# Kernel optimization log

Measured on AMD Instinct MI355X. Metric: run time of the kernel, lower is better.

The kernel has to match this reference:

```python
import jax, jax.numpy as jnp
import numpy as np

N_NODES = 100000
N_EDGES = 1600000
D_IN, D_HID, D_OUT = 256, 512, 48
K_STEPS = 10
ALPHA = 0.1


def setup_inputs() -> dict:
    key = jax.random.key(0)
    k_x, k_e, k_w1, k_w2 = jax.random.split(key, 4)
    x = jax.random.normal(k_x, (N_NODES, D_IN), dtype=jnp.float32)
    edge_index = jax.random.randint(k_e, (2, N_EDGES), 0, N_NODES, dtype=jnp.int64)
    # MLP params (Kaiming-ish scaling)
    W1 = jax.random.normal(k_w1, (D_IN, D_HID), dtype=jnp.float32) * (1.0 / np.sqrt(D_IN))
    b1 = jnp.zeros((D_HID,), dtype=jnp.float32)
    W2 = jax.random.normal(k_w2, (D_HID, D_OUT), dtype=jnp.float32) * (1.0 / np.sqrt(D_HID))
    b2 = jnp.zeros((D_OUT,), dtype=jnp.float32)
    return {"x": x, "edge_index": edge_index, "W1": W1, "b1": b1, "W2": W2, "b2": b2}


def reference(x, edge_index, W1, b1, W2, b2):
    N = x.shape[0]
    # --- MLP encoder ---
    h = jax.nn.relu(x @ W1 + b1) @ W2 + b2  # [N, D_OUT]

    # --- APPNP propagation (PyG defaults: add self-loops, symmetric gcn_norm) ---
    loop = jnp.arange(N, dtype=edge_index.dtype)
    src = jnp.concatenate([edge_index[0], loop])  # [E+N]
    dst = jnp.concatenate([edge_index[1], loop])
    ones = jnp.ones(src.shape[0], dtype=h.dtype)
    deg = jax.ops.segment_sum(ones, dst, num_segments=N)  # in-degree incl. self-loop
    dinv = jnp.where(deg > 0, jax.lax.rsqrt(deg), 0.0)
    norm = dinv[src] * dinv[dst]  # [E+N]

    out = h
    for _ in range(K_STEPS):
        msg = out[src] * norm[:, None]                      # gather + scale
        agg = jax.ops.segment_sum(msg, dst, num_segments=N)  # scatter-add
        out = (1.0 - ALPHA) * agg + ALPHA * h                # teleport mix
    return out
```

## Files before the change

### kernel.cpp

```cpp
#include <hip/hip_runtime.h>
#include <hip/hip_fp16.h>

constexpr int D_IN = 256, D_HID = 512, D_OUT = 48;
constexpr int HPAD = 64;
constexpr int K_STEPS = 10;

typedef __attribute__((ext_vector_type(8))) __bf16 bf16x8;
typedef __attribute__((ext_vector_type(4))) float f32x4;

__device__ __forceinline__ unsigned short f2bf(float f) {
  unsigned u = __builtin_bit_cast(unsigned, f);
  u += 0x7fffu + ((u >> 16) & 1u);
  return (unsigned short)(u >> 16);
}

__device__ __forceinline__ void gl2lds16(const unsigned short* g, unsigned short* l) {
  __builtin_amdgcn_global_load_lds(
      (const __attribute__((address_space(1))) unsigned int*)g,
      (__attribute__((address_space(3))) unsigned int*)l, 16, 0, 0);
}


__global__ void zero2_kernel(int* __restrict__ a, int* __restrict__ b, int N) {
  int i = blockIdx.x * 256 + threadIdx.x;
  if (i < N) { a[i] = 0; b[i] = 0; }
}

__global__ void count_kernel(const int* __restrict__ dst, int* __restrict__ cnt, int E) {
  int e = blockIdx.x * 256 + threadIdx.x;
  if (e < E) atomicAdd(&cnt[dst[e]], 1);
}

__global__ void dinv_kernel(const int* __restrict__ cnt, float* __restrict__ dinv, int N) {
  int n = blockIdx.x * 256 + threadIdx.x;
  if (n < N) dinv[n] = rsqrtf((float)(cnt[n] + 1));
}

__global__ void scan1_kernel(const int* __restrict__ cnt, int* __restrict__ row_ptr,
                             int* __restrict__ bsum, int N) {
  __shared__ int sd[256];
  int tid = threadIdx.x, b = blockIdx.x;
  int i0 = b * 1024 + tid * 4;
  int v[4];
#pragma unroll
  for (int m = 0; m < 4; ++m) v[m] = (i0 + m < N) ? ((cnt[i0 + m] + 3) & ~3) : 0;
  int s = v[0] + v[1] + v[2] + v[3];
  sd[tid] = s;
  __syncthreads();
  for (int off = 1; off < 256; off <<= 1) {
    int t = (tid >= off) ? sd[tid - off] : 0;
    __syncthreads();
    sd[tid] += t;
    __syncthreads();
  }
  int run = sd[tid] - s;
#pragma unroll
  for (int m = 0; m < 4; ++m) {
    if (i0 + m < N) row_ptr[i0 + m] = run;
    run += v[m];
  }
  if (tid == 255) bsum[b] = sd[255];
}

__global__ void scan2_kernel(const int* __restrict__ bsum, int* __restrict__ bofs,
                             int* __restrict__ row_ptr, int NB, int N) {
  __shared__ int sd[128];
  int tid = threadIdx.x;
  int v = (tid < NB) ? bsum[tid] : 0;
  sd[tid] = v;
  __syncthreads();
  for (int off = 1; off < 128; off <<= 1) {
    int t = (tid >= off) ? sd[tid - off] : 0;
    __syncthreads();
    sd[tid] += t;
    __syncthreads();
  }
  if (tid < NB) bofs[tid] = sd[tid] - v;
  if (tid == 127) row_ptr[N] = sd[127];
}

__global__ void scan3_kernel(int* __restrict__ row_ptr, const int* __restrict__ bofs, int N) {
  int b = blockIdx.x;
  if (b == 0) return;
  int add = bofs[b];
  int i0 = b * 1024 + threadIdx.x * 4;
#pragma unroll
  for (int m = 0; m < 4; ++m)
    if (i0 + m < N) row_ptr[i0 + m] += add;
}

__global__ void fill_kernel(const int* __restrict__ src, const int* __restrict__ dst,
                            const int* __restrict__ row_ptr, int* __restrict__ cnt2,
                            const float* __restrict__ dinv,
                            int2* __restrict__ edges, int E) {
  int e = blockIdx.x * 256 + threadIdx.x;
  if (e >= E) return;
  int s = src[e], d = dst[e];
  int p = row_ptr[d] + atomicAdd(&cnt2[d], 1);
  edges[p] = make_int2(s, __float_as_int(dinv[s]));
}

__global__ void pad_kernel(const int* __restrict__ cnt, const int* __restrict__ row_ptr,
                           int2* __restrict__ edges, int N) {
  int n = blockIdx.x * 256 + threadIdx.x;
  if (n >= N) return;
  int a = row_ptr[n] + cnt[n];
  int b = row_ptr[n + 1];
  for (int p = a; p < b; ++p) edges[p] = make_int2(n, 0);
}


__global__ void convert_w1(const float* __restrict__ W1, unsigned short* __restrict__ W1F) {
  int i = blockIdx.x * 256 + threadIdx.x;
  if (i >= D_HID * D_IN) return;
  int c = i >> 8, k = i & 255;
  int ct = c >> 6, tn = (c >> 4) & 3, l15 = c & 15;
  int kb = k >> 5, q = (k >> 3) & 3, j = k & 7;
  int lane = (q << 4) | l15;
  int dst = (((ct * 4 + tn) * 8 + kb) << 9) + lane * 8 + j;
  W1F[dst] = f2bf(W1[k * D_HID + c]);
}

__global__ void convert_w2(const float* __restrict__ W2, unsigned short* __restrict__ W2F) {
  int i = blockIdx.x * 256 + threadIdx.x;
  if (i >= D_OUT * D_HID) return;
  int n = i >> 9, k = i & 511;
  int ct = k >> 6, kk = (k >> 5) & 1, q = (k >> 3) & 3, j = k & 7;
  int tn = n >> 4, l15 = n & 15;
  int lane = (q << 4) | l15;
  int dst = (((ct * 2 + kk) * 3 + tn) << 9) + lane * 8 + j;
  W2F[dst] = f2bf(W2[k * D_OUT + n]);
}


__global__ __launch_bounds__(256, 3) void encoder_kernel(
    const float* __restrict__ x, const float* __restrict__ b1,
    const float* __restrict__ b2,
    const unsigned short* __restrict__ W1F,
    const unsigned short* __restrict__ W2F,
    __half* __restrict__ h2, int N) {
  __shared__ unsigned short sW1[16384];
  __shared__ unsigned short sHid[4][2][16][72];

  int tid = threadIdx.x;
  int w = tid >> 6, lane = tid & 63;
  int q = lane >> 4, l15 = lane & 15;
  int row0 = blockIdx.x * 128 + w * 32;

  uint4 axu[2][8];
#pragma unroll
  for (int mt = 0; mt < 2; ++mt) {
    int grow = row0 + mt * 16 + l15;
    bool rok = grow < N;
    const float* xr = x + (size_t)grow * D_IN;
#pragma unroll
    for (int jb = 0; jb < 8; ++jb) {
      float4 v0 = make_float4(0.f, 0.f, 0.f, 0.f), v1 = v0;
      if (rok) {
        v0 = *(const float4*)(xr + jb * 32 + q * 8);
        v1 = *(const float4*)(xr + jb * 32 + q * 8 + 4);
      }
      union { uint4 u; unsigned short s[8]; } uu;
      uu.s[0] = f2bf(v0.x); uu.s[1] = f2bf(v0.y); uu.s[2] = f2bf(v0.z); uu.s[3] = f2bf(v0.w);
      uu.s[4] = f2bf(v1.x); uu.s[5] = f2bf(v1.y); uu.s[6] = f2bf(v1.z); uu.s[7] = f2bf(v1.w);
      axu[mt][jb] = uu.u;
    }
  }

  f32x4 hacc[2][3];
#pragma unroll
  for (int mt = 0; mt < 2; ++mt)
#pragma unroll
    for (int t = 0; t < 3; ++t)
#pragma unroll
      for (int r = 0; r < 4; ++r) hacc[mt][t][r] = 0.f;

  for (int ct = 0; ct < 8; ++ct) {
    int c0 = ct * 64;
    __syncthreads();
    {
      const unsigned short* gsrc = W1F + ((size_t)ct << 14) + (w << 9) + lane * 8;
      unsigned short* ldst = &sW1[w << 9];
#pragma unroll
      for (int i = 0; i < 8; ++i)
        gl2lds16(gsrc + (i << 11), ldst + (i << 11));
    }
    __syncthreads();

    f32x4 acc[2][4];
#pragma unroll
    for (int mt = 0; mt < 2; ++mt)
#pragma unroll
      for (int t = 0; t < 4; ++t)
#pragma unroll
        for (int r = 0; r < 4; ++r) acc[mt][t][r] = 0.f;

    const unsigned short* sb = &sW1[lane * 8];
#pragma unroll
    for (int kb = 0; kb < 8; ++kb) {
      bf16x8 bq0 = *(const bf16x8*)(sb + (kb << 9));
      bf16x8 bq1 = *(const bf16x8*)(sb + (kb << 9) + 4096);
      bf16x8 bq2 = *(const bf16x8*)(sb + (kb << 9) + 8192);
      bf16x8 bq3 = *(const bf16x8*)(sb + (kb << 9) + 12288);
      bf16x8 a0 = __builtin_bit_cast(bf16x8, axu[0][kb]);
      bf16x8 a1 = __builtin_bit_cast(bf16x8, axu[1][kb]);
      acc[0][0] = __builtin_amdgcn_mfma_f32_16x16x32_bf16(a0, bq0, acc[0][0], 0, 0, 0);
      acc[1][0] = __builtin_amdgcn_mfma_f32_16x16x32_bf16(a1, bq0, acc[1][0], 0, 0, 0);
      acc[0][1] = __builtin_amdgcn_mfma_f32_16x16x32_bf16(a0, bq1, acc[0][1], 0, 0, 0);
      acc[1][1] = __builtin_amdgcn_mfma_f32_16x16x32_bf16(a1, bq1, acc[1][1], 0, 0, 0);
      acc[0][2] = __builtin_amdgcn_mfma_f32_16x16x32_bf16(a0, bq2, acc[0][2], 0, 0, 0);
      acc[1][2] = __builtin_amdgcn_mfma_f32_16x16x32_bf16(a1, bq2, acc[1][2], 0, 0, 0);
      acc[0][3] = __builtin_amdgcn_mfma_f32_16x16x32_bf16(a0, bq3, acc[0][3], 0, 0, 0);
      acc[1][3] = __builtin_amdgcn_mfma_f32_16x16x32_bf16(a1, bq3, acc[1][3], 0, 0, 0);
    }
#pragma unroll
    for (int mt = 0; mt < 2; ++mt)
#pragma unroll
      for (int tn = 0; tn < 4; ++tn) {
        int c = tn * 16 + l15;
        float bias = b1[c0 + c];
#pragma unroll
        for (int rg = 0; rg < 4; ++rg) {
          float v = acc[mt][tn][rg] + bias;
          v = v > 0.f ? v : 0.f;
          sHid[w][mt][q * 4 + rg][c] = f2bf(v);
        }
      }
#pragma unroll
    for (int kk = 0; kk < 2; ++kk) {
      bf16x8 a0 = *(const bf16x8*)&sHid[w][0][l15][kk * 32 + q * 8];
      bf16x8 a1 = *(const bf16x8*)&sHid[w][1][l15][kk * 32 + q * 8];
      const unsigned short* w2b = W2F + (((ct * 2 + kk) * 3) << 9) + lane * 8;
#pragma unroll
      for (int tn = 0; tn < 3; ++tn) {
        bf16x8 b = *(const bf16x8*)(w2b + (tn << 9));
        hacc[0][tn] = __builtin_amdgcn_mfma_f32_16x16x32_bf16(a0, b, hacc[0][tn], 0, 0, 0);
        hacc[1][tn] = __builtin_amdgcn_mfma_f32_16x16x32_bf16(a1, b, hacc[1][tn], 0, 0, 0);
      }
    }
  }
#pragma unroll
  for (int mt = 0; mt < 2; ++mt) {
#pragma unroll
    for (int tn = 0; tn < 3; ++tn) {
      int c = tn * 16 + l15;
      float bias = b2[c];
#pragma unroll
      for (int rg = 0; rg < 4; ++rg) {
        int gr = row0 + mt * 16 + q * 4 + rg;
        if (gr < N) h2[(size_t)gr * HPAD + c] = __float2half(hacc[mt][tn][rg] + bias);
      }
    }
#pragma unroll
    for (int rg = 0; rg < 4; ++rg) {
      int gr = row0 + mt * 16 + q * 4 + rg;
      if (gr < N) h2[(size_t)gr * HPAD + 48 + l15] = __float2half(0.f);
    }
  }
}


__global__ __launch_bounds__(256) void prop_kernel(
    const __half* __restrict__ cur, const __half* __restrict__ h2,
    const float* __restrict__ dinv, const int* __restrict__ row_ptr,
    const int2* __restrict__ edges, __half* __restrict__ nxt,
    float* __restrict__ outf, int N, int last) {
  int wid = (blockIdx.x * 256 + threadIdx.x) >> 6;
  int lane = threadIdx.x & 63;
  int half = lane >> 5;
  int slot = (lane >> 3) & 3;
  int s = lane & 7;
  int node = wid * 2 + half;
  bool nok = node < N;
  int p0 = 0, p1 = 0;
  if (nok) { int2 pp = *(const int2*)(row_ptr + node); p0 = pp.x; p1 = pp.y; }
  int d = p1 - p0;
  int dmax = max(d, __shfl_xor(d, 32));
  int nb = dmax >> 2;

  float acc[8];
#pragma unroll
  for (int i = 0; i < 8; ++i) acc[i] = 0.f;

  int p = p0 + slot;
  int2 e0 = make_int2(0, 0), e1 = make_int2(0, 0);
  if (nb > 0) e0 = edges[p];
  if (nb > 1) e1 = edges[p + 4];
  int b = 0;
  for (; b + 2 <= nb; b += 2) {
    int2 n0 = make_int2(0, 0), n1 = make_int2(0, 0);
    if (b + 2 < nb) n0 = edges[p + 8];
    if (b + 3 < nb) n1 = edges[p + 12];
    float w0 = (p < p1) ? __int_as_float(e0.y) : 0.f;
    float w1 = (p + 4 < p1) ? __int_as_float(e1.y) : 0.f;
    union { float4 f; __half2 h[4]; } u0, u1;
    u0.f = *(const float4*)(cur + ((size_t)e0.x << 6) + s * 8);
    u1.f = *(const float4*)(cur + ((size_t)e1.x << 6) + s * 8);
#pragma unroll
    for (int i = 0; i < 4; ++i) {
      float2 f0 = __half22float2(u0.h[i]);
      float2 f1 = __half22float2(u1.h[i]);
      acc[2 * i]     += w0 * f0.x + w1 * f1.x;
      acc[2 * i + 1] += w0 * f0.y + w1 * f1.y;
    }
    e0 = n0; e1 = n1; p += 8;
  }
  if (b < nb) {
    float w0 = (p < p1) ? __int_as_float(e0.y) : 0.f;
    union { float4 f; __half2 h[4]; } u0;
    u0.f = *(const float4*)(cur + ((size_t)e0.x << 6) + s * 8);
#pragma unroll
    for (int i = 0; i < 4; ++i) {
      float2 f0 = __half22float2(u0.h[i]);
      acc[2 * i]     += w0 * f0.x;
      acc[2 * i + 1] += w0 * f0.y;
    }
  }
#pragma unroll
  for (int i = 0; i < 8; ++i) {
    acc[i] += __int_as_float(__builtin_amdgcn_ds_swizzle(__float_as_int(acc[i]), 0x201F));
    acc[i] += __int_as_float(__builtin_amdgcn_ds_swizzle(__float_as_int(acc[i]), 0x401F));
  }
  if ((lane & 24) != 0 || !nok) return;
  float di = dinv[node];
  size_t base = ((size_t)node << 6) + s * 8;
  union { float4 f; __half2 h[4]; } us, uh;
  us.f = *(const float4*)(cur + base);
  uh.f = *(const float4*)(h2 + base);
  float dii = di * di;
  float outv[8];
#pragma unroll
  for (int i = 0; i < 4; ++i) {
    float2 sf = __half22float2(us.h[i]);
    float2 hf = __half22float2(uh.h[i]);
    outv[2 * i]     = 0.9f * (di * acc[2 * i]     + dii * sf.x) + 0.1f * hf.x;
    outv[2 * i + 1] = 0.9f * (di * acc[2 * i + 1] + dii * sf.y) + 0.1f * hf.y;
  }
  if (last) {
    if (s < 6) {
      float* op = outf + (size_t)node * D_OUT + s * 8;
      *(float4*)op       = make_float4(outv[0], outv[1], outv[2], outv[3]);
      *(float4*)(op + 4) = make_float4(outv[4], outv[5], outv[6], outv[7]);
    }
  } else {
    union { uint4 u4; __half2 h[4]; } o;
#pragma unroll
    for (int i = 0; i < 4; ++i) o.h[i] = __floats2half2_rn(outv[2 * i], outv[2 * i + 1]);
    *(uint4*)(nxt + base) = o.u4;
  }
}


extern "C" void kernel_launch(void* const* d_in, const int* in_sizes, int n_in,
                              void* d_out, int out_size, void* d_ws, size_t ws_size,
                              hipStream_t stream) {
  (void)n_in; (void)out_size; (void)ws_size;
  const float* x  = (const float*)d_in[0];
  const int*   ei = (const int*)d_in[1];
  const float* W1 = (const float*)d_in[2];
  const float* b1 = (const float*)d_in[3];
  const float* W2 = (const float*)d_in[4];
  const float* b2 = (const float*)d_in[5];
  const int N = in_sizes[0] / D_IN;
  const int E = in_sizes[1] / 2;
  const int* e_src = ei;
  const int* e_dst = ei + E;

  char* ws = (char*)d_ws;
  size_t off = 0;
  auto take = [&](size_t bytes) -> char* {
    char* p = ws + off;
    off += (bytes + 511) & ~(size_t)511;
    return p;
  };
  int* cnt      = (int*)take((size_t)N * 4);
  int* cnt2     = (int*)take((size_t)N * 4);
  float* dinv   = (float*)take((size_t)N * 4);
  int* row_ptr  = (int*)take((size_t)(N + 1) * 4);
  int* bsum     = (int*)take(1024);
  int* bofs     = (int*)take(1024);
  int2* edges   = (int2*)take(((size_t)E + 4 * (size_t)N) * 8);
  unsigned short* W1F = (unsigned short*)take((size_t)D_IN * D_HID * 2);
  unsigned short* W2F = (unsigned short*)take((size_t)D_HID * D_OUT * 2);
  __half* h2    = (__half*)take((size_t)N * HPAD * 2);
  __half* bufA  = (__half*)take((size_t)N * HPAD * 2);
  __half* bufB  = (__half*)d_out;
  float* outp   = (float*)d_out;

  int nb256 = (N + 255) / 256;
  int eb256 = (E + 255) / 256;
  int NB    = (N + 1023) / 1024;

  zero2_kernel<<<nb256, 256, 0, stream>>>(cnt, cnt2, N);
  count_kernel<<<eb256, 256, 0, stream>>>(e_dst, cnt, E);
  dinv_kernel<<<nb256, 256, 0, stream>>>(cnt, dinv, N);
  scan1_kernel<<<NB, 256, 0, stream>>>(cnt, row_ptr, bsum, N);
  scan2_kernel<<<1, 128, 0, stream>>>(bsum, bofs, row_ptr, NB, N);
  scan3_kernel<<<NB, 256, 0, stream>>>(row_ptr, bofs, N);
  fill_kernel<<<eb256, 256, 0, stream>>>(e_src, e_dst, row_ptr, cnt2, dinv, edges, E);
  pad_kernel<<<nb256, 256, 0, stream>>>(cnt, row_ptr, edges, N);

  convert_w1<<<(D_IN * D_HID + 255) / 256, 256, 0, stream>>>(W1, W1F);
  convert_w2<<<(D_HID * D_OUT + 255) / 256, 256, 0, stream>>>(W2, W2F);
  encoder_kernel<<<(N + 127) / 128, 256, 0, stream>>>(x, b1, b2, W1F, W2F, h2, N);

  int waves = (N + 1) / 2;
  int pblocks = (waves + 3) / 4;
  const __half* src = h2;
  __half* dst = bufA;
  for (int it = 1; it <= K_STEPS; ++it) {
    int last = (it == K_STEPS);
    prop_kernel<<<pblocks, 256, 0, stream>>>(src, h2, dinv, row_ptr, edges,
                                             dst, outp, N, last);
    src = dst;
    dst = (dst == bufA) ? bufB : bufA;
  }
}
```

Measured before the change: 713.4 us.

## Partition atomic CSR build by destination range and retile encoder to 512 threads

The count and fill kernels now use a fixed grid of 2048 blocks split into 8 teams. Each team scans every edge but only performs atomics for destinations in its own 4096-node band, to improve atomic locality in L2. The encoder switches to 512-thread blocks with one 16-row tile per wave, caches the biases in LDS, and preloads the first W1 chunk before the x loads. In exchange, every edge is read 8 times in count and fill, and the W1 reload now sits between barriers without a double buffer.

Measured after the change: 714.8 us. About the same (+0.2%).

```diff
diff --git a/kernel.cpp b/kernel.cpp
--- a/kernel.cpp
+++ b/kernel.cpp
@@ -26,9 +26,15 @@
   if (i < N) { a[i] = 0; b[i] = 0; }
 }
 
-__global__ void count_kernel(const int* __restrict__ dst, int* __restrict__ cnt, int E) {
-  int e = blockIdx.x * 256 + threadIdx.x;
-  if (e < E) atomicAdd(&cnt[dst[e]], 1);
+__global__ __launch_bounds__(256) void count_kernel(const int* __restrict__ dst,
+                                                    int* __restrict__ cnt, int E) {
+  int team = blockIdx.x & 7;
+  int bt = blockIdx.x >> 3;
+  int step = (gridDim.x >> 3) * 256;
+  for (int e = bt * 256 + threadIdx.x; e < E; e += step) {
+    int d = dst[e];
+    if (((d >> 12) & 7) == team) atomicAdd(&cnt[d], 1);
+  }
 }
 
 __global__ void dinv_kernel(const int* __restrict__ cnt, float* __restrict__ dinv, int N) {
@@ -89,15 +95,20 @@
     if (i0 + m < N) row_ptr[i0 + m] += add;
 }
 
-__global__ void fill_kernel(const int* __restrict__ src, const int* __restrict__ dst,
-                            const int* __restrict__ row_ptr, int* __restrict__ cnt2,
-                            const float* __restrict__ dinv,
-                            int2* __restrict__ edges, int E) {
-  int e = blockIdx.x * 256 + threadIdx.x;
-  if (e >= E) return;
-  int s = src[e], d = dst[e];
-  int p = row_ptr[d] + atomicAdd(&cnt2[d], 1);
-  edges[p] = make_int2(s, __float_as_int(dinv[s]));
+__global__ __launch_bounds__(256) void fill_kernel(
+    const int* __restrict__ src, const int* __restrict__ dst,
+    const int* __restrict__ row_ptr, int* __restrict__ cnt2,
+    const float* __restrict__ dinv, int2* __restrict__ edges, int E) {
+  int team = blockIdx.x & 7;
+  int bt = blockIdx.x >> 3;
+  int step = (gridDim.x >> 3) * 256;
+  for (int e = bt * 256 + threadIdx.x; e < E; e += step) {
+    int d = dst[e];
+    if (((d >> 12) & 7) != team) continue;
+    int s = src[e];
+    int p = row_ptr[d] + atomicAdd(&cnt2[d], 1);
+    edges[p] = make_int2(s, __float_as_int(dinv[s]));
+  }
 }
 
 __global__ void pad_kernel(const int* __restrict__ cnt, const int* __restrict__ row_ptr,
@@ -133,129 +144,127 @@
 }
 
 
-__global__ __launch_bounds__(256, 3) void encoder_kernel(
+__global__ __launch_bounds__(512, 4) void encoder_kernel(
     const float* __restrict__ x, const float* __restrict__ b1,
     const float* __restrict__ b2,
     const unsigned short* __restrict__ W1F,
     const unsigned short* __restrict__ W2F,
     __half* __restrict__ h2, int N) {
   __shared__ unsigned short sW1[16384];
-  __shared__ unsigned short sHid[4][2][16][72];
+  __shared__ unsigned short sHid[8][16][72];
+  __shared__ float sB1[512];
+  __shared__ float sB2[64];
 
   int tid = threadIdx.x;
   int w = tid >> 6, lane = tid & 63;
   int q = lane >> 4, l15 = lane & 15;
-  int row0 = blockIdx.x * 128 + w * 32;
-
-  uint4 axu[2][8];
-#pragma unroll
-  for (int mt = 0; mt < 2; ++mt) {
-    int grow = row0 + mt * 16 + l15;
-    bool rok = grow < N;
-    const float* xr = x + (size_t)grow * D_IN;
-#pragma unroll
-    for (int jb = 0; jb < 8; ++jb) {
-      float4 v0 = make_float4(0.f, 0.f, 0.f, 0.f), v1 = v0;
-      if (rok) {
-        v0 = *(const float4*)(xr + jb * 32 + q * 8);
-        v1 = *(const float4*)(xr + jb * 32 + q * 8 + 4);
-      }
-      union { uint4 u; unsigned short s[8]; } uu;
-      uu.s[0] = f2bf(v0.x); uu.s[1] = f2bf(v0.y); uu.s[2] = f2bf(v0.z); uu.s[3] = f2bf(v0.w);
-      uu.s[4] = f2bf(v1.x); uu.s[5] = f2bf(v1.y); uu.s[6] = f2bf(v1.z); uu.s[7] = f2bf(v1.w);
-      axu[mt][jb] = uu.u;
-    }
-  }
-
-  f32x4 hacc[2][3];
-#pragma unroll
-  for (int mt = 0; mt < 2; ++mt)
-#pragma unroll
-    for (int t = 0; t < 3; ++t)
-#pragma unroll
-      for (int r = 0; r < 4; ++r) hacc[mt][t][r] = 0.f;
+  int row0 = blockIdx.x * 128 + w * 16;
+
+  {
+    const unsigned short* gsrc = W1F + (w << 9) + lane * 8;
+    unsigned short* ldst = &sW1[w << 9];
+#pragma unroll
+    for (int i = 0; i < 4; ++i)
+      gl2lds16(gsrc + (i << 12), ldst + (i << 12));
+  }
+  sB1[tid] = b1[tid];
+  if (tid < 48) sB2[tid] = b2[tid];
+
+  int grow = row0 + l15;
+  bool rok = grow < N;
+  const float* xr = x + (size_t)grow * D_IN;
+  float4 xv[16];
+#pragma unroll
+  for (int jb = 0; jb < 8; ++jb) {
+    xv[2 * jb]     = rok ? *(const float4*)(xr + jb * 32 + q * 8)
+                         : make_float4(0.f, 0.f, 0.f, 0.f);
+    xv[2 * jb + 1] = rok ? *(const float4*)(xr + jb * 32 + q * 8 + 4)
+                         : make_float4(0.f, 0.f, 0.f, 0.f);
+  }
+  uint4 axu[8];
+#pragma unroll
+  for (int jb = 0; jb < 8; ++jb) {
+    union { uint4 u; unsigned short s[8]; } uu;
+    float4 v0 = xv[2 * jb], v1 = xv[2 * jb + 1];
+    uu.s[0] = f2bf(v0.x); uu.s[1] = f2bf(v0.y); uu.s[2] = f2bf(v0.z); uu.s[3] = f2bf(v0.w);
+    uu.s[4] = f2bf(v1.x); uu.s[5] = f2bf(v1.y); uu.s[6] = f2bf(v1.z); uu.s[7] = f2bf(v1.w);
+    axu[jb] = uu.u;
+  }
+
+  f32x4 hacc[3];
+#pragma unroll
+  for (int t = 0; t < 3; ++t)
+#pragma unroll
+    for (int r = 0; r < 4; ++r) hacc[t][r] = 0.f;
+
+  __syncthreads();
 
   for (int ct = 0; ct < 8; ++ct) {
     int c0 = ct * 64;
-    __syncthreads();
-    {
-      const unsigned short* gsrc = W1F + ((size_t)ct << 14) + (w << 9) + lane * 8;
-      unsigned short* ldst = &sW1[w << 9];
-#pragma unroll
-      for (int i = 0; i < 8; ++i)
-        gl2lds16(gsrc + (i << 11), ldst + (i << 11));
-    }
-    __syncthreads();
-
-    f32x4 acc[2][4];
-#pragma unroll
-    for (int mt = 0; mt < 2; ++mt)
-#pragma unroll
-      for (int t = 0; t < 4; ++t)
-#pragma unroll
-        for (int r = 0; r < 4; ++r) acc[mt][t][r] = 0.f;
+    f32x4 acc[4];
+#pragma unroll
+    for (int t = 0; t < 4; ++t)
+#pragma unroll
+      for (int r = 0; r < 4; ++r) acc[t][r] = 0.f;
 
     const unsigned short* sb = &sW1[lane * 8];
 #pragma unroll
     for (int kb = 0; kb < 8; ++kb) {
+      bf16x8 a = __builtin_bit_cast(bf16x8, axu[kb]);
       bf16x8 bq0 = *(const bf16x8*)(sb + (kb << 9));
       bf16x8 bq1 = *(const bf16x8*)(sb + (kb << 9) + 4096);
       bf16x8 bq2 = *(const bf16x8*)(sb + (kb << 9) + 8192);
       bf16x8 bq3 = *(const bf16x8*)(sb + (kb << 9) + 12288);
-      bf16x8 a0 = __builtin_bit_cast(bf16x8, axu[0][kb]);
-      bf16x8 a1 = __builtin_bit_cast(bf16x8, axu[1][kb]);
-      acc[0][0] = __builtin_amdgcn_mfma_f32_16x16x32_bf16(a0, bq0, acc[0][0], 0, 0, 0);
-      acc[1][0] = __builtin_amdgcn_mfma_f32_16x16x32_bf16(a1, bq0, acc[1][0], 0, 0, 0);
-      acc[0][1] = __builtin_amdgcn_mfma_f32_16x16x32_bf16(a0, bq1, acc[0][1], 0, 0, 0);
-      acc[1][1] = __builtin_amdgcn_mfma_f32_16x16x32_bf16(a1, bq1, acc[1][1], 0, 0, 0);
-      acc[0][2] = __builtin_amdgcn_mfma_f32_16x16x32_bf16(a0, bq2, acc[0][2], 0, 0, 0);
-      acc[1][2] = __builtin_amdgcn_mfma_f32_16x16x32_bf16(a1, bq2, acc[1][2], 0, 0, 0);
-      acc[0][3] = __builtin_amdgcn_mfma_f32_16x16x32_bf16(a0, bq3, acc[0][3], 0, 0, 0);
-      acc[1][3] = __builtin_amdgcn_mfma_f32_16x16x32_bf16(a1, bq3, acc[1][3], 0, 0, 0);
-    }
-#pragma unroll
-    for (int mt = 0; mt < 2; ++mt)
-#pragma unroll
-      for (int tn = 0; tn < 4; ++tn) {
-        int c = tn * 16 + l15;
-        float bias = b1[c0 + c];
-#pragma unroll
-        for (int rg = 0; rg < 4; ++rg) {
-          float v = acc[mt][tn][rg] + bias;
-          v = v > 0.f ? v : 0.f;
-          sHid[w][mt][q * 4 + rg][c] = f2bf(v);
-        }
+      acc[0] = __builtin_amdgcn_mfma_f32_16x16x32_bf16(a, bq0, acc[0], 0, 0, 0);
+      acc[1] = __builtin_amdgcn_mfma_f32_16x16x32_bf16(a, bq1, acc[1], 0, 0, 0);
+      acc[2] = __builtin_amdgcn_mfma_f32_16x16x32_bf16(a, bq2, acc[2], 0, 0, 0);
+      acc[3] = __builtin_amdgcn_mfma_f32_16x16x32_bf16(a, bq3, acc[3], 0, 0, 0);
+    }
+#pragma unroll
+    for (int tn = 0; tn < 4; ++tn) {
+      int c = tn * 16 + l15;
+      float bias = sB1[c0 + c];
+#pragma unroll
+      for (int rg = 0; rg < 4; ++rg) {
+        float v = acc[tn][rg] + bias;
+        v = v > 0.f ? v : 0.f;
+        sHid[w][q * 4 + rg][c] = f2bf(v);
       }
+    }
 #pragma unroll
     for (int kk = 0; kk < 2; ++kk) {
-      bf16x8 a0 = *(const bf16x8*)&sHid[w][0][l15][kk * 32 + q * 8];
-      bf16x8 a1 = *(const bf16x8*)&sHid[w][1][l15][kk * 32 + q * 8];
+      bf16x8 a0 = *(const bf16x8*)&sHid[w][l15][kk * 32 + q * 8];
       const unsigned short* w2b = W2F + (((ct * 2 + kk) * 3) << 9) + lane * 8;
 #pragma unroll
       for (int tn = 0; tn < 3; ++tn) {
         bf16x8 b = *(const bf16x8*)(w2b + (tn << 9));
-        hacc[0][tn] = __builtin_amdgcn_mfma_f32_16x16x32_bf16(a0, b, hacc[0][tn], 0, 0, 0);
-        hacc[1][tn] = __builtin_amdgcn_mfma_f32_16x16x32_bf16(a1, b, hacc[1][tn], 0, 0, 0);
+        hacc[tn] = __builtin_amdgcn_mfma_f32_16x16x32_bf16(a0, b, hacc[tn], 0, 0, 0);
       }
     }
-  }
-#pragma unroll
-  for (int mt = 0; mt < 2; ++mt) {
-#pragma unroll
-    for (int tn = 0; tn < 3; ++tn) {
-      int c = tn * 16 + l15;
-      float bias = b2[c];
-#pragma unroll
-      for (int rg = 0; rg < 4; ++rg) {
-        int gr = row0 + mt * 16 + q * 4 + rg;
-        if (gr < N) h2[(size_t)gr * HPAD + c] = __float2half(hacc[mt][tn][rg] + bias);
-      }
-    }
+    __syncthreads();
+    if (ct < 7) {
+      const unsigned short* gsrc = W1F + ((size_t)(ct + 1) << 14) + (w << 9) + lane * 8;
+      unsigned short* ldst = &sW1[w << 9];
+#pragma unroll
+      for (int i = 0; i < 4; ++i)
+        gl2lds16(gsrc + (i << 12), ldst + (i << 12));
+      __syncthreads();
+    }
+  }
+#pragma unroll
+  for (int tn = 0; tn < 3; ++tn) {
+    int c = tn * 16 + l15;
+    float bias = sB2[c];
 #pragma unroll
     for (int rg = 0; rg < 4; ++rg) {
-      int gr = row0 + mt * 16 + q * 4 + rg;
-      if (gr < N) h2[(size_t)gr * HPAD + 48 + l15] = __float2half(0.f);
-    }
+      int gr = row0 + q * 4 + rg;
+      if (gr < N) h2[(size_t)gr * HPAD + c] = __float2half(hacc[tn][rg] + bias);
+    }
+  }
+#pragma unroll
+  for (int rg = 0; rg < 4; ++rg) {
+    int gr = row0 + q * 4 + rg;
+    if (gr < N) h2[(size_t)gr * HPAD + 48 + l15] = __float2half(0.f);
   }
 }
 
@@ -392,17 +401,17 @@
   int NB    = (N + 1023) / 1024;
 
   zero2_kernel<<<nb256, 256, 0, stream>>>(cnt, cnt2, N);
-  count_kernel<<<eb256, 256, 0, stream>>>(e_dst, cnt, E);
+  count_kernel<<<2048, 256, 0, stream>>>(e_dst, cnt, E);
   dinv_kernel<<<nb256, 256, 0, stream>>>(cnt, dinv, N);
   scan1_kernel<<<NB, 256, 0, stream>>>(cnt, row_ptr, bsum, N);
   scan2_kernel<<<1, 128, 0, stream>>>(bsum, bofs, row_ptr, NB, N);
   scan3_kernel<<<NB, 256, 0, stream>>>(row_ptr, bofs, N);
-  fill_kernel<<<eb256, 256, 0, stream>>>(e_src, e_dst, row_ptr, cnt2, dinv, edges, E);
+  fill_kernel<<<2048, 256, 0, stream>>>(e_src, e_dst, row_ptr, cnt2, dinv, edges, E);
   pad_kernel<<<nb256, 256, 0, stream>>>(cnt, row_ptr, edges, N);
 
   convert_w1<<<(D_IN * D_HID + 255) / 256, 256, 0, stream>>>(W1, W1F);
   convert_w2<<<(D_HID * D_OUT + 255) / 256, 256, 0, stream>>>(W2, W2F);
-  encoder_kernel<<<(N + 127) / 128, 256, 0, stream>>>(x, b1, b2, W1F, W2F, h2, N);
+  encoder_kernel<<<(N + 127) / 128, 512, 0, stream>>>(x, b1, b2, W1F, W2F, h2, N);
 
   int waves = (N + 1) / 2;
   int pblocks = (waves + 3) / 4;
```
